# Optimization experiments

Hardware: AMD Instinct MI355X
Metric: run time of the kernel (lower is better)

## Reference

```python
import jax, jax.numpy as jnp
import numpy as np

L = 2
S = (L + 1) ** 2            # 9 spherical harmonic coefficients
C = 128                     # sphere_channels
H = 128                     # hidden_channels
NH = 8                      # num_heads
A = 32                      # attn_alpha_channels
V = 16                      # attn_value_channels
N = 5000                    # nodes
E = 50000                   # edges
DE = 128                    # invariant edge embedding dim
G = 18                      # S2 grid points

# l of each coefficient in l-major layout [S]
L_OF = np.concatenate([np.full(2 * l + 1, l) for l in range(L + 1)])
IDX_M0 = np.array([l * l + l for l in range(L + 1)])

def _idx_m(m):
    neg = np.array([l * l + l - m for l in range(m, L + 1)])
    pos = np.array([l * l + l + m for l in range(m, L + 1)])
    return neg, pos

IDX_M1_NEG, IDX_M1_POS = _idx_m(1)
IDX_M2_NEG, IDX_M2_POS = _idx_m(2)
# m-major ordering and its inverse permutation back to l-major
PERM = np.concatenate([IDX_M0, IDX_M1_POS, IDX_M1_NEG, IDX_M2_POS, IDX_M2_NEG])
INV_PERM = np.argsort(PERM)


def _silu(x):
    return x * jax.nn.sigmoid(x)


def _layernorm(x, g, b, eps=1e-5):
    mu = x.mean(-1, keepdims=True)
    var = ((x - mu) ** 2).mean(-1, keepdims=True)
    return (x - mu) * jax.lax.rsqrt(var + eps) * g + b


def _smooth_leaky_relu(x, a=0.2):
    return 0.5 * (1 + a) * x + 0.5 * (1 - a) * x * (2 * jax.nn.sigmoid(x) - 1)


def _so2_conv(x, w_m0, b_m0, w_m1, w_m2, cout):
    """SO(2) convolution on rotated embeddings. x: [E,S,Cin] l-major.
    Returns ([E,S,cout] l-major, extra m=0 channels)."""
    e = x.shape[0]
    # m = 0: plain linear over flattened (L+1)*Cin
    x0 = x[:, IDX_M0, :].reshape(e, -1)
    y0 = x0 @ w_m0 + b_m0
    y0_main = y0[:, : (L + 1) * cout].reshape(e, L + 1, cout)
    y0_extra = y0[:, (L + 1) * cout:]
    parts = [y0_main]
    # m > 0: complex (cos/sin) SO2 mixing with shared weight for real/imag
    for neg, pos, w in ((IDX_M1_NEG, IDX_M1_POS, w_m1), (IDX_M2_NEG, IDX_M2_POS, w_m2)):
        nl = len(neg)
        xr = x[:, pos, :].reshape(e, -1)
        xi = x[:, neg, :].reshape(e, -1)
        yr = xr @ w  # [E, 2*nl*cout]
        yi = xi @ w
        yr_r, yr_i = yr[:, : nl * cout], yr[:, nl * cout:]
        yi_r, yi_i = yi[:, : nl * cout], yi[:, nl * cout:]
        parts.append((yr_r - yi_i).reshape(e, nl, cout))   # +m (real)
        parts.append((yr_i + yi_r).reshape(e, nl, cout))   # -m (imag)
    out_m = jnp.concatenate(parts, axis=1)                 # m-major
    return out_m[:, INV_PERM, :], y0_extra


def _s2_act(x, togrid, fromgrid):
    g = jnp.einsum('gs,esc->egc', togrid, x)
    return jnp.einsum('sg,egc->esc', fromgrid, _silu(g))


def _sep_s2_act(scalars, x, togrid, fromgrid):
    t = _s2_act(x, togrid, fromgrid)
    return jnp.concatenate([_silu(scalars)[:, None, :], t[:, 1:, :]], axis=1)


def _so3_linear(x, w, b):
    # w: [L+1, Cin, Cout], shared across m within each l; bias only on l=0
    out = jnp.einsum('nsc,sco->nso', x, w[L_OF])
    return out.at[:, 0, :].add(b)


def _eqv_norm(x, g, b, eps=1e-5):
    # l=0: layernorm over channels; l>0: RMS over (m, channels) per degree
    outs = [_layernorm(x[:, 0:1, :], g[0], b)]
    for l in range(1, L + 1):
        sl = x[:, l * l:(l + 1) * (l + 1), :]
        rms = jnp.sqrt(jnp.mean(sl ** 2, axis=(1, 2), keepdims=True) + eps)
        outs.append(sl / rms * g[l])
    return jnp.concatenate(outs, axis=1)


def _forward(x, edge_distance, wigner, rad_w1, rad_b1, rad_ln_g, rad_ln_b, rad_w2, rad_b2,
             w1_m0, b1_m0, w1_m1, w1_m2, w2_m0, b2_m0, w2_m1, w2_m2,
             alpha_ln_g, alpha_ln_b, alpha_dot, proj_w, proj_b,
             norm1_g, norm1_b, norm2_g, norm2_b,
             gate_w, gate_b, ffn_w1, ffn_b1, ffn_w2, ffn_b2,
             togrid, fromgrid, edge_src, edge_dst):
    # ---------- SO2 equivariant graph attention ----------
    xn = _eqv_norm(x, norm1_g, norm1_b)
    msg = jnp.concatenate([xn[edge_src], xn[edge_dst]], axis=-1)      # [E,S,2C]
    msg = jnp.einsum('eij,ejc->eic', wigner, msg)                     # rotate to edge frame
    # radial function shared across m within each l (use_m_share_rad)
    h = _silu(_layernorm(edge_distance @ rad_w1 + rad_b1, rad_ln_g, rad_ln_b))
    rad = (h @ rad_w2 + rad_b2).reshape(-1, L + 1, 2 * C)             # [E,L+1,2C]
    msg = msg * rad[:, L_OF, :]
    hid, x0_extra = _so2_conv(msg, w1_m0, b1_m0, w1_m1, w1_m2, H)
    x_alpha = x0_extra[:, : NH * A].reshape(-1, NH, A)
    gating = x0_extra[:, NH * A:]                                     # [E,H]
    hid = _sep_s2_act(gating, hid, togrid, fromgrid)
    val, _ = _so2_conv(hid, w2_m0, b2_m0, w2_m1, w2_m2, NH * V)
    val = jnp.einsum('eji,ejc->eic', wigner, val)                     # rotate back (D^T)
    # attention weights with per-destination segment softmax
    a = _smooth_leaky_relu(_layernorm(x_alpha, alpha_ln_g, alpha_ln_b))
    a = jnp.einsum('eha,ha->eh', a, alpha_dot)                        # [E,NH]
    amax = jax.ops.segment_max(a, edge_dst, num_segments=N)
    aexp = jnp.exp(a - amax[edge_dst])
    asum = jax.ops.segment_sum(aexp, edge_dst, num_segments=N)
    attn = aexp / asum[edge_dst]
    msg_out = (val.reshape(-1, S, NH, V) * attn[:, None, :, None]).reshape(-1, S, NH * V)
    node = jax.ops.segment_sum(msg_out, edge_dst, num_segments=N)     # [N,S,NH*V]
    x = x + _so3_linear(node, proj_w, proj_b)
    # ---------- spherical FFN (sep S2 gating) ----------
    xn = _eqv_norm(x, norm2_g, norm2_b)
    gating = xn[:, 0, :] @ gate_w + gate_b
    hh = _so3_linear(xn, ffn_w1, ffn_b1)
    hh = _sep_s2_act(gating, hh, togrid, fromgrid)
    return x + _so3_linear(hh, ffn_w2, ffn_b2)


def setup_inputs() -> dict:
    key = jax.random.key(0)
    ks = iter(jax.random.split(key, 64))
    def nrm(shape, scale=1.0):
        return jax.random.normal(next(ks), shape, dtype=jnp.float32) * scale
    EX = NH * A + H
    inp = {}
    inp['x'] = nrm((N, S, C))
    inp['edge_distance'] = nrm((E, DE))
    inp['wigner'] = nrm((E, S, S), 1.0 / np.sqrt(S))
    inp['rad_w1'] = nrm((DE, 64), 1.0 / np.sqrt(DE)); inp['rad_b1'] = jnp.zeros((64,), jnp.float32)
    inp['rad_ln_g'] = jnp.ones((64,), jnp.float32); inp['rad_ln_b'] = jnp.zeros((64,), jnp.float32)
    inp['rad_w2'] = nrm((64, 2 * C * (L + 1)), 0.05); inp['rad_b2'] = jnp.ones((2 * C * (L + 1),), jnp.float32)
    inp['w1_m0'] = nrm(((L + 1) * 2 * C, (L + 1) * H + EX), 1.0 / np.sqrt((L + 1) * 2 * C))
    inp['b1_m0'] = jnp.zeros(((L + 1) * H + EX,), jnp.float32)
    inp['w1_m1'] = nrm((2 * 2 * C, 2 * 2 * H), 1.0 / np.sqrt(2 * 2 * C))
    inp['w1_m2'] = nrm((2 * C, 2 * H), 1.0 / np.sqrt(2 * C))
    inp['w2_m0'] = nrm(((L + 1) * H, (L + 1) * NH * V), 1.0 / np.sqrt((L + 1) * H))
    inp['b2_m0'] = jnp.zeros(((L + 1) * NH * V,), jnp.float32)
    inp['w2_m1'] = nrm((2 * H, 2 * 2 * NH * V), 1.0 / np.sqrt(2 * H))
    inp['w2_m2'] = nrm((H, 2 * NH * V), 1.0 / np.sqrt(H))
    inp['alpha_ln_g'] = jnp.ones((A,), jnp.float32); inp['alpha_ln_b'] = jnp.zeros((A,), jnp.float32)
    inp['alpha_dot'] = nrm((NH, A), 1.0 / np.sqrt(A))
    inp['proj_w'] = nrm((L + 1, NH * V, C), 1.0 / np.sqrt(NH * V)); inp['proj_b'] = jnp.zeros((C,), jnp.float32)
    inp['norm1_g'] = jnp.ones((L + 1, C), jnp.float32); inp['norm1_b'] = jnp.zeros((C,), jnp.float32)
    inp['norm2_g'] = jnp.ones((L + 1, C), jnp.float32); inp['norm2_b'] = jnp.zeros((C,), jnp.float32)
    inp['gate_w'] = nrm((C, H), 1.0 / np.sqrt(C)); inp['gate_b'] = jnp.zeros((H,), jnp.float32)
    inp['ffn_w1'] = nrm((L + 1, C, H), 1.0 / np.sqrt(C)); inp['ffn_b1'] = jnp.zeros((H,), jnp.float32)
    inp['ffn_w2'] = nrm((L + 1, H, C), 1.0 / np.sqrt(H)); inp['ffn_b2'] = jnp.zeros((C,), jnp.float32)
    inp['togrid'] = nrm((G, S), 1.0 / np.sqrt(S))
    inp['fromgrid'] = nrm((S, G), 1.0 / np.sqrt(G))
    inp['edge_src'] = jax.random.randint(next(ks), (E,), 0, N)
    inp['edge_dst'] = jax.random.randint(next(ks), (E,), 0, N)
    return inp


def reference(x, edge_distance, wigner, rad_w1, rad_b1, rad_ln_g, rad_ln_b, rad_w2, rad_b2,
              w1_m0, b1_m0, w1_m1, w1_m2, w2_m0, b2_m0, w2_m1, w2_m2,
              alpha_ln_g, alpha_ln_b, alpha_dot, proj_w, proj_b,
              norm1_g, norm1_b, norm2_g, norm2_b,
              gate_w, gate_b, ffn_w1, ffn_b1, ffn_w2, ffn_b2,
              togrid, fromgrid, edge_src, edge_dst):
    return _forward(x, edge_distance, wigner, rad_w1, rad_b1, rad_ln_g, rad_ln_b, rad_w2, rad_b2,
                    w1_m0, b1_m0, w1_m1, w1_m2, w2_m0, b2_m0, w2_m1, w2_m2,
                    alpha_ln_g, alpha_ln_b, alpha_dot, proj_w, proj_b,
                    norm1_g, norm1_b, norm2_g, norm2_b,
                    gate_w, gate_b, ffn_w1, ffn_b1, ffn_w2, ffn_b2,
                    togrid, fromgrid, edge_src, edge_dst)
```

## Files before the change

### kernel.cpp

```cpp
#include <hip/hip_runtime.h>
#include <hip/hip_bf16.h>

typedef unsigned short u16;
typedef unsigned int   u32;
typedef __attribute__((ext_vector_type(8))) short short8;
typedef __attribute__((ext_vector_type(4))) float float4v;

#define NN 5000
#define EE 50000

__device__ __forceinline__ float b2f(u16 u){ return __uint_as_float(((u32)u)<<16); }
__device__ __forceinline__ u16 f2b(float f){
  u32 x = __float_as_uint(f);
  u32 r = (x + 0x7fffu + ((x>>16)&1u)) >> 16;
  return (u16)r;
}
__device__ __forceinline__ float ldin(const void* p, size_t i, bool f32){
  return f32 ? ((const float*)p)[i] : b2f(((const u16*)p)[i]);
}
__device__ __forceinline__ float siluf(float x){ return x/(1.f+__expf(-x)); }
__device__ __forceinline__ float waveRedSum(float v){
  #pragma unroll
  for (int m=32;m>=1;m>>=1) v += __shfl_xor(v,m,64);
  return v;
}
__device__ __forceinline__ float red32(float v){
  #pragma unroll
  for (int m=16;m>=1;m>>=1) v += __shfl_xor(v,m,64);
  return v;
}
__device__ __forceinline__ void gload_lds16(const u16* g, u16* l){
  __builtin_amdgcn_global_load_lds((const __attribute__((address_space(1))) void*)g,
                                   (__attribute__((address_space(3))) void*)l, 16, 0, 0);
}


__global__ __launch_bounds__(256) void zero_kernel(float* __restrict__ p, int n){
  for (int i = blockIdx.x*256 + threadIdx.x; i < n; i += gridDim.x*256) p[i] = 0.f;
}

__global__ void detect_kernel(const u32* __restrict__ ng, int* __restrict__ flag){
  if (blockIdx.x == 0 && threadIdx.x == 0) *flag = (ng[0] == 0x3F800000u) ? 1 : 0;
}

__global__ __launch_bounds__(256) void hist_kernel(const int* __restrict__ edst,
    int* __restrict__ counts){
  int e = blockIdx.x*256 + threadIdx.x;
  if (e < EE) atomicAdd(&counts[edst[e]], 1);
}

__global__ __launch_bounds__(1024) void scan_kernel(const int* __restrict__ counts,
    int* __restrict__ row_start, int* __restrict__ cursor){
  __shared__ int buf[1024];
  __shared__ int base;
  const int t = threadIdx.x;
  if (t == 0){ base = 0; row_start[0] = 0; }
  __syncthreads();
  for (int i0 = 0; i0 < NN; i0 += 1024){
    int i = i0 + t;
    int c = (i < NN) ? counts[i] : 0;
    buf[t] = c;
    __syncthreads();
    #pragma unroll
    for (int ofs = 1; ofs < 1024; ofs <<= 1){
      int v = (t >= ofs) ? buf[t-ofs] : 0;
      __syncthreads();
      buf[t] += v;
      __syncthreads();
    }
    if (i < NN){
      int incl = base + buf[t];
      row_start[i+1] = incl;
      cursor[i] = incl - c;
    }
    __syncthreads();
    if (t == 0) base += buf[1023];
    __syncthreads();
  }
}

__global__ __launch_bounds__(256) void place_kernel(const int* __restrict__ edst,
    int* __restrict__ cursor, int* __restrict__ order){
  int e = blockIdx.x*256 + threadIdx.x;
  if (e < EE) order[atomicAdd(&cursor[edst[e]], 1)] = e;
}

__global__ __launch_bounds__(256) void cvt_kernel(const int* __restrict__ dflag,
    const void* __restrict__ src, long long off0, u16* __restrict__ dst, int n){
  const bool f32 = (*dflag != 0);
  for (int i = blockIdx.x*256 + threadIdx.x; i < n; i += gridDim.x*256)
    dst[i] = f32 ? f2b(((const float*)src)[off0 + i]) : ((const u16*)src)[off0 + i];
}

__global__ __launch_bounds__(256) void gathercvt_kernel(const int* __restrict__ dflag,
    const void* __restrict__ src, const int* __restrict__ order, int e0,
    u16* __restrict__ dst, int n){
  const bool f32 = (*dflag != 0);
  for (int i = blockIdx.x*256 + threadIdx.x; i < n; i += gridDim.x*256){
    int le = i >> 7, c = i & 127;
    int eg = order[e0 + le];
    dst[i] = f2b(ldin(src, (size_t)eg*128 + c, f32));
  }
}

__global__ __launch_bounds__(256) void biasprep_kernel(const int* __restrict__ dflag,
    const void* b1,const void* b2,const void* rb1,const void* rb2,
    const void* pb,const void* gb,const void* f1,const void* f2,
    u16* d_b1,u16* d_b2,u16* d_rb1,u16* d_rb2,u16* d_pb,u16* d_gb,u16* d_f1,u16* d_f2){
  const bool f32 = (*dflag != 0);
  int t = blockIdx.x*256 + threadIdx.x;
  if (t < 768) d_b1[t]  = f2b(ldin(b1, t, f32));
  if (t < 384) d_b2[t]  = f2b(ldin(b2, t, f32));
  if (t < 64)  d_rb1[t] = f2b(ldin(rb1, t, f32));
  if (t < 768) d_rb2[t] = f2b(ldin(rb2, t, f32));
  if (t < 128){
    d_pb[t] = f2b(ldin(pb, t, f32));
    d_gb[t] = f2b(ldin(gb, t, f32));
    d_f1[t] = f2b(ldin(f1, t, f32));
    d_f2[t] = f2b(ldin(f2, t, f32));
  }
}

__global__ __launch_bounds__(256) void cvtT_kernel(const int* __restrict__ dflag,
    const void* __restrict__ src, long long off0, u16* __restrict__ dst, int K, int N){
  const bool f32 = (*dflag != 0);
  int total = K*N;
  for (int i = blockIdx.x*256 + threadIdx.x; i < total; i += gridDim.x*256){
    int n = i / K, k = i % K;
    dst[i] = f2b(ldin(src, (size_t)off0 + (size_t)k*N + n, f32));
  }
}

__global__ __launch_bounds__(256) void cvtT3_kernel(const int* __restrict__ dflag,
    const void* __restrict__ src, u16* __restrict__ dst){
  const bool f32 = (*dflag != 0);
  const long long l = blockIdx.y;
  for (int i = blockIdx.x*256 + threadIdx.x; i < 16384; i += gridDim.x*256){
    int n = i >> 7, k = i & 127;
    dst[l*16384 + i] = f2b(ldin(src, (size_t)l*16384 + (size_t)k*128 + n, f32));
  }
}

__global__ __launch_bounds__(256) void wprepT_kernel(const int* __restrict__ dflag,
    const void* __restrict__ w, u16* __restrict__ wt, int K0, int N0){
  const bool f32 = (*dflag != 0);
  int total = 2*N0*2*K0;
  for (int i = blockIdx.x*blockDim.x + threadIdx.x; i < total; i += gridDim.x*blockDim.x){
    int c = i / (2*K0), r = i % (2*K0);
    float v;
    if (r < K0) v = ldin(w, (size_t)r*2*N0 + c, f32);
    else {
      int rr = r - K0;
      if (c < N0) v = -ldin(w, (size_t)rr*2*N0 + N0 + c, f32);
      else        v =  ldin(w, (size_t)rr*2*N0 + (c - N0), f32);
    }
    wt[i] = f2b(v);
  }
}

__global__ __launch_bounds__(128) void eqvnorm_kernel(const int* __restrict__ dflag,
    const void* __restrict__ x, int in_always_f32,
    const void* __restrict__ g, const void* __restrict__ b,
    void* __restrict__ out, int out_f32){
  const bool f32 = (*dflag != 0);
  const bool inf32 = in_always_f32 || f32;
  const int n = blockIdx.x, t = threadIdx.x;
  __shared__ float red[2];
  float v[9];
  #pragma unroll
  for (int s=0;s<9;s++) v[s] = ldin(x, (size_t)n*1152 + s*128 + t, inf32);

  auto bsum = [&](float val)->float{
    float w = waveRedSum(val);
    __syncthreads();
    if ((t & 63) == 0) red[t>>6] = w;
    __syncthreads();
    return red[0] + red[1];
  };
  auto store = [&](int idx, float val){
    if (out_f32) ((float*)out)[(size_t)n*1152 + idx] = val;
    else         ((u16*) out)[(size_t)n*1152 + idx] = f2b(val);
  };
  float mu  = bsum(v[0]) * (1.f/128.f);
  float d0  = v[0] - mu;
  float var = bsum(d0*d0) * (1.f/128.f);
  store(t, d0 * rsqrtf(var + 1e-5f) * ldin(g, t, f32) + ldin(b, t, f32));
  float ss1 = v[1]*v[1] + v[2]*v[2] + v[3]*v[3];
  float inv1 = rsqrtf(bsum(ss1)*(1.f/384.f) + 1e-5f);
  float g1 = ldin(g, 128 + t, f32);
  #pragma unroll
  for (int s=1;s<=3;s++) store(s*128 + t, v[s]*inv1*g1);
  float ss2 = 0.f;
  #pragma unroll
  for (int s=4;s<9;s++) ss2 += v[s]*v[s];
  float inv2 = rsqrtf(bsum(ss2)*(1.f/640.f) + 1e-5f);
  float g2 = ldin(g, 256 + t, f32);
  #pragma unroll
  for (int s=4;s<9;s++) store(s*128 + t, v[s]*inv2*g2);
}

__global__ __launch_bounds__(256) void gemm_mfma_kernel(
    const u16* __restrict__ A, int lda, int K,
    const u16* __restrict__ Wt, int NOUT,
    const u16* __restrict__ bias,
    u16* __restrict__ out0, int ld0, int coloff0, int split,
    u16* __restrict__ out1, int ld1, int M){
  __shared__ __align__(16) u16 As[2][128*32];
  __shared__ __align__(16) u16 Bs[2][128*32];
  const int t = threadIdx.x;
  const int r0 = blockIdx.x * 128;
  const int n0 = blockIdx.y * 128;
  const int lane = t & 63, wave = t >> 6;
  const int wr = (wave & 1) * 64, wn = (wave >> 1) * 64;
  float4v acc[4][4];
  #pragma unroll
  for (int i=0;i<4;i++)
    #pragma unroll
    for (int j=0;j<4;j++) acc[i][j] = (float4v){0.f,0.f,0.f,0.f};

  const int fr = lane & 15, fq = (lane >> 4) * 8;

  const int Rw   = wave * 32;
  const int srow = lane >> 2;
  const int scol = (lane & 3) * 8;
  const u16* aG0 = A  + (size_t)(r0 + Rw + srow) * lda + scol;
  const u16* aG1 = aG0 + (size_t)16 * lda;
  const bool aV0 = (r0 + Rw + srow)      < M;
  const bool aV1 = (r0 + Rw + 16 + srow) < M;
  const u16* bG0 = Wt + (size_t)(n0 + Rw + srow) * K + scol;
  const u16* bG1 = bG0 + (size_t)16 * K;
  const bool bV0 = (n0 + Rw + srow)      < NOUT;
  const bool bV1 = (n0 + Rw + 16 + srow) < NOUT;

  auto stage = [&](int buf, int k0){
    u16* lA = &As[buf][Rw * 32];
    u16* lB = &Bs[buf][Rw * 32];
    if (aV0) gload_lds16(aG0 + k0, lA);
    if (aV1) gload_lds16(aG1 + k0, lA + 16*32);
    if (bV0) gload_lds16(bG0 + k0, lB);
    if (bV1) gload_lds16(bG1 + k0, lB + 16*32);
  };

  stage(0, 0);
  __syncthreads();
  int cur = 0;
  for (int k0 = 0; k0 < K; k0 += 32){
    const int k1 = k0 + 32;
    if (k1 < K) stage(cur ^ 1, k1);
    short8 af[4], bfv[4];
    #pragma unroll
    for (int i=0;i<4;i++){
      af[i]  = *(const short8*)&As[cur][(wr + i*16 + fr)*32 + fq];
      bfv[i] = *(const short8*)&Bs[cur][(wn + i*16 + fr)*32 + fq];
    }
    #pragma unroll
    for (int i=0;i<4;i++)
      #pragma unroll
      for (int j=0;j<4;j++)
        acc[i][j] = __builtin_amdgcn_mfma_f32_16x16x32_bf16(af[i], bfv[j], acc[i][j], 0, 0, 0);
    __syncthreads();
    cur ^= 1;
  }
  const int quad = lane >> 4;
  #pragma unroll
  for (int j=0;j<4;j++){
    int col = n0 + wn + j*16 + fr;
    if (col >= NOUT) continue;
    float bv = bias ? b2f(bias[col]) : 0.f;
    #pragma unroll
    for (int i=0;i<4;i++){
      int rbase = r0 + wr + i*16 + quad*4;
      #pragma unroll
      for (int rg=0; rg<4; rg++){
        int row = rbase + rg;
        if (row >= M) continue;
        float v = acc[i][j][rg] + bv;
        if (col < split) out0[(size_t)row*ld0 + coloff0 + col] = f2b(v);
        else             out1[(size_t)row*ld1 + (col - split)] = f2b(v);
      }
    }
  }
}

__global__ __launch_bounds__(256) void gemm_node_kernel(
    const int* __restrict__ dflag,
    const u16* __restrict__ A,
    const u16* __restrict__ W3t,
    const u16* __restrict__ bias,
    const void* __restrict__ resid, int resid_mode,
    void* __restrict__ out, int out_mode, int gate_out){
  const bool f32 = (*dflag != 0);
  const int l = blockIdx.y;
  const int rpn  = (l==0) ? 1 : ((l==1) ? 3 : 5);
  const int soff = (l==0) ? 0 : ((l==1) ? 1 : 4);
  const int M = NN * rpn;
  const int r0 = blockIdx.x * 128;
  if (r0 >= M) return;
  __shared__ __align__(16) u16 As[128][40];
  __shared__ __align__(16) u16 Bs[128][40];
  const int t = threadIdx.x;
  const int lane = t & 63, wave = t >> 6;
  const int wr = (wave & 1) * 64, wn = (wave >> 1) * 64;
  float4v acc[4][4];
  #pragma unroll
  for (int i=0;i<4;i++)
    #pragma unroll
    for (int j=0;j<4;j++) acc[i][j] = (float4v){0.f,0.f,0.f,0.f};

  const int sr = t >> 2, sc = (t & 3) * 8;
  const int fr = lane & 15, fq = (lane >> 4) * 8;
  size_t abase[2]; bool aval[2];
  #pragma unroll
  for (int s2=0;s2<2;s2++){
    int m = r0 + sr + s2*64;
    aval[s2] = m < M;
    int n = m / rpn, srow = soff + (m % rpn);
    abase[s2] = (size_t)n*1152 + srow*128 + sc;
  }
  const u16* Wl = W3t + (size_t)l*16384;

  #pragma unroll
  for (int k0 = 0; k0 < 128; k0 += 32){
    #pragma unroll
    for (int s2=0;s2<2;s2++){
      int row = sr + s2*64;
      uint4 av = make_uint4(0u,0u,0u,0u);
      if (aval[s2]) av = *(const uint4*)(A + abase[s2] + k0);
      *(uint4*)&As[row][sc] = av;
      uint4 wv = *(const uint4*)(Wl + (size_t)row*128 + k0 + sc);
      *(uint4*)&Bs[row][sc] = wv;
    }
    __syncthreads();
    short8 af[4], bfr[4];
    #pragma unroll
    for (int i=0;i<4;i++){
      af[i]  = *(const short8*)&As[wr + i*16 + fr][fq];
      bfr[i] = *(const short8*)&Bs[wn + i*16 + fr][fq];
    }
    #pragma unroll
    for (int i=0;i<4;i++)
      #pragma unroll
      for (int j=0;j<4;j++)
        acc[i][j] = __builtin_amdgcn_mfma_f32_16x16x32_bf16(af[i], bfr[j], acc[i][j], 0, 0, 0);
    __syncthreads();
  }
  const int quad = lane >> 4;
  #pragma unroll
  for (int j=0;j<4;j++){
    int col = wn + j*16 + fr;
    float bv = (bias && l==0) ? b2f(bias[col]) : 0.f;
    #pragma unroll
    for (int i=0;i<4;i++){
      int rbase = r0 + wr + i*16 + quad*4;
      #pragma unroll
      for (int rg=0; rg<4; rg++){
        int m = rbase + rg;
        if (m >= M) continue;
        int n = m / rpn, srow = soff + (m % rpn);
        size_t na = (size_t)n*1152 + srow*128 + col;
        float v = acc[i][j][rg] + bv;
        if (resid_mode == 1)      v += ((const float*)resid)[na];
        else if (resid_mode == 2) v += ldin(resid, na, f32);
        if (gate_out)            ((u16*)out)[(size_t)n*128 + col] = f2b(v);
        else if (out_mode == 0)  ((u16*)out)[na] = f2b(v);
        else if (out_mode == 1)  ((float*)out)[na] = v;
        else { if (f32) ((float*)out)[na] = v; else ((u16*)out)[na] = f2b(v); }
      }
    }
  }
}

__global__ __launch_bounds__(256) void nodecvt_kernel(const float* __restrict__ node,
    const float* __restrict__ nsum, u16* __restrict__ nodeb){
  for (int i = blockIdx.x*256 + threadIdx.x; i < NN*1152; i += gridDim.x*256){
    int n = i / 1152, c = i & 127, h = c >> 4;
    float ns = nsum[(size_t)n*8 + h];
    float rs = (ns > 0.f) ? 1.f/ns : 0.f;
    nodeb[i] = f2b(node[i] * rs);
  }
}

__global__ __launch_bounds__(128) void node_s2act_kernel(const int* __restrict__ dflag,
    const u16* __restrict__ hh, const u16* __restrict__ gating,
    const void* __restrict__ tg, const void* __restrict__ fg, u16* __restrict__ hh2){
  const bool f32 = (*dflag != 0);
  const int n = blockIdx.x, t = threadIdx.x;
  __shared__ float TG[162], FG[162];
  for (int i=t; i<162; i+=128){ TG[i]=ldin(tg,i,f32); FG[i]=ldin(fg,i,f32); }
  float hv[9];
  #pragma unroll
  for (int s=0;s<9;s++) hv[s] = b2f(hh[(size_t)n*1152 + s*128 + t]);
  __syncthreads();
  float gg[18];
  #pragma unroll
  for (int gi=0;gi<18;gi++){
    float a = 0.f;
    #pragma unroll
    for (int s=0;s<9;s++) a = fmaf(TG[gi*9+s], hv[s], a);
    gg[gi] = siluf(a);
  }
  hh2[(size_t)n*1152 + t] = f2b(siluf(b2f(gating[(size_t)n*128 + t])));
  #pragma unroll
  for (int s=1;s<9;s++){
    float a = 0.f;
    #pragma unroll
    for (int gi=0;gi<18;gi++) a = fmaf(FG[s*18+gi], gg[gi], a);
    hh2[(size_t)n*1152 + s*128 + t] = f2b(a);
  }
}

__global__ __launch_bounds__(256) void lnsilu_kernel(const int* __restrict__ dflag,
    u16* __restrict__ H, const void* __restrict__ rlng, const void* __restrict__ rlnb, int M){
  const bool f32 = (*dflag != 0);
  const int r = blockIdx.x*4 + (threadIdx.x >> 6), lane = threadIdx.x & 63;
  if (r >= M) return;
  float h = b2f(H[(size_t)r*64 + lane]);
  float mu = waveRedSum(h) * (1.f/64.f);
  float d = h - mu;
  float var = waveRedSum(d*d) * (1.f/64.f);
  float hn = d * rsqrtf(var + 1e-5f) * ldin(rlng, lane, f32) + ldin(rlnb, lane, f32);
  H[(size_t)r*64 + lane] = f2b(siluf(hn));
}

__global__ __launch_bounds__(256) void edge_rot_kernel(const int* __restrict__ dflag,
    const u16* __restrict__ xn, const void* __restrict__ wig,
    const u16* __restrict__ rad,
    const int* __restrict__ esrc, const int* __restrict__ edst,
    const int* __restrict__ order, int e0, u16* __restrict__ msg){
  const bool f32 = (*dflag != 0);
  const int le = blockIdx.x, t = threadIdx.x;
  const int eg = order[e0 + le];
  __shared__ float W[81];
  if (t < 81) W[t] = ldin(wig, (size_t)eg*81 + t, f32);
  const int src = esrc[eg], dst = edst[eg];
  float pre[9];
  const u16* base = (t < 128) ? (xn + (size_t)src*1152 + t) : (xn + (size_t)dst*1152 + (t-128));
  #pragma unroll
  for (int j=0;j<9;j++) pre[j] = b2f(base[j*128]);
  __syncthreads();
  float rot[9];
  #pragma unroll
  for (int i=0;i<9;i++){
    float a = 0.f;
    #pragma unroll
    for (int j=0;j<9;j++) a = fmaf(W[i*9+j], pre[j], a);
    rot[i] = a;
  }
  float r[3];
  #pragma unroll
  for (int l=0;l<3;l++) r[l] = b2f(rad[(size_t)le*768 + l*256 + t]);
  const int INVP[9] = {0,5,1,3,8,6,2,4,7};
  const int LOF[9]  = {0,1,1,1,2,2,2,2,2};
  u16* mb = msg + (size_t)le*2304 + t;
  #pragma unroll
  for (int i=0;i<9;i++) mb[INVP[i]*256] = f2b(rot[i] * r[LOF[i]]);
}

__global__ __launch_bounds__(256) void s2act_alpha_kernel(const int* __restrict__ dflag,
    const u16* __restrict__ hid, const u16* __restrict__ extra,
    const void* __restrict__ togrid, const void* __restrict__ fromgrid,
    const void* __restrict__ alng, const void* __restrict__ alnb, const void* __restrict__ adot,
    const int* __restrict__ edst, const int* __restrict__ order, int e0,
    u16* __restrict__ hid2, float* __restrict__ aexp, float* __restrict__ nsum){
  const bool f32 = (*dflag != 0);
  const int le = blockIdx.x, t = threadIdx.x;
  const int p = e0 + le;
  __shared__ float TG[162], FG[162];
  if (t < 162){ TG[t] = ldin(togrid, t, f32); FG[t] = ldin(fromgrid, t, f32); }
  {
    const int h = t >> 5, ai = t & 31;
    float v = b2f(extra[(size_t)le*384 + t]);
    float mu = red32(v) * (1.f/32.f);
    float d = v - mu;
    float var = red32(d*d) * (1.f/32.f);
    float xh = d * rsqrtf(var + 1e-5f) * ldin(alng, ai, f32) + ldin(alnb, ai, f32);
    float sig = 1.f/(1.f + __expf(-xh));
    float sl = 0.6f*xh + 0.4f*xh*(2.f*sig - 1.f);
    float pp = sl * ldin(adot, h*32 + ai, f32);
    float dot = red32(pp);
    if (ai == 0){
      float ex = __expf(dot - 8.f);
      aexp[(size_t)p*8 + h] = ex;
      atomicAdd(&nsum[(size_t)edst[order[p]]*8 + h], ex);
    }
  }
  __syncthreads();
  if (t < 128){
    const int INVP[9] = {0,5,1,3,8,6,2,4,7};
    float hv[9];
    #pragma unroll
    for (int s=0;s<9;s++) hv[s] = b2f(hid[(size_t)le*1152 + INVP[s]*128 + t]);
    float gg[18];
    #pragma unroll
    for (int gi=0;gi<18;gi++){
      float a = 0.f;
      #pragma unroll
      for (int s=0;s<9;s++) a = fmaf(TG[gi*9+s], hv[s], a);
      gg[gi] = siluf(a);
    }
    hid2[(size_t)le*1152 + t] = f2b(siluf(b2f(extra[(size_t)le*384 + 256 + t])));
    #pragma unroll
    for (int s=1;s<9;s++){
      float a = 0.f;
      #pragma unroll
      for (int gi=0;gi<18;gi++) a = fmaf(FG[s*18+gi], gg[gi], a);
      hid2[(size_t)le*1152 + INVP[s]*128 + t] = f2b(a);
    }
  }
}

__global__ __launch_bounds__(128) void unrot_gather_kernel(const int* __restrict__ dflag,
    const u16* __restrict__ val, const void* __restrict__ wig,
    const float* __restrict__ aexp, const int* __restrict__ order,
    const int* __restrict__ row_start, int e0, int Mc, float* __restrict__ node){
  const bool f32 = (*dflag != 0);
  const int n = blockIdx.x, t = threadIdx.x;
  const int s = row_start[n], tend = row_start[n+1];
  int lo = (s > e0) ? s : e0;
  int hi = (tend < e0 + Mc) ? tend : (e0 + Mc);
  if (lo >= hi) return;
  __shared__ float W[81];
  __shared__ float SC[8];
  const int INVP[9] = {0,5,1,3,8,6,2,4,7};
  float acc[9];
  #pragma unroll
  for (int i=0;i<9;i++) acc[i] = 0.f;
  for (int p = lo; p < hi; p++){
    const int le = p - e0;
    const int eg = order[p];
    __syncthreads();
    if (t < 81) W[t] = ldin(wig, (size_t)eg*81 + t, f32);
    if (t >= 120) SC[t-120] = aexp[(size_t)p*8 + (t-120)];
    __syncthreads();
    float vs[9];
    #pragma unroll
    for (int j=0;j<9;j++) vs[j] = b2f(val[(size_t)le*1152 + INVP[j]*128 + t]);
    const float sc = SC[t>>4];
    #pragma unroll
    for (int i=0;i<9;i++){
      float a = 0.f;
      #pragma unroll
      for (int j=0;j<9;j++) a = fmaf(W[j*9+i], vs[j], a);
      acc[i] = fmaf(a, sc, acc[i]);
    }
  }
  const bool full = (s >= e0) && (tend <= e0 + Mc);
  #pragma unroll
  for (int i=0;i<9;i++){
    float* dst = &node[(size_t)n*1152 + i*128 + t];
    if (full) *dst = acc[i];
    else      atomicAdd(dst, acc[i]);
  }
}

extern "C" void kernel_launch(void* const* d_in, const int* in_sizes, int n_in,
                              void* d_out, int out_size, void* d_ws, size_t ws_size,
                              hipStream_t stream){
  (void)in_sizes; (void)n_in; (void)out_size;
  const void* x       = d_in[0];
  const void* edist   = d_in[1];
  const void* wig     = d_in[2];
  const void* rad_w1  = d_in[3];
  const void* rad_b1  = d_in[4];
  const void* rad_lng = d_in[5];
  const void* rad_lnb = d_in[6];
  const void* rad_w2  = d_in[7];
  const void* rad_b2  = d_in[8];
  const void* w1_m0   = d_in[9];
  const void* b1_m0   = d_in[10];
  const void* w1_m1   = d_in[11];
  const void* w1_m2   = d_in[12];
  const void* w2_m0   = d_in[13];
  const void* b2_m0   = d_in[14];
  const void* w2_m1   = d_in[15];
  const void* w2_m2   = d_in[16];
  const void* alng    = d_in[17];
  const void* alnb    = d_in[18];
  const void* adot    = d_in[19];
  const void* proj_w  = d_in[20];
  const void* proj_b  = d_in[21];
  const void* norm1_g = d_in[22];
  const void* norm1_b = d_in[23];
  const void* norm2_g = d_in[24];
  const void* norm2_b = d_in[25];
  const void* gate_w  = d_in[26];
  const void* gate_b  = d_in[27];
  const void* ffn_w1  = d_in[28];
  const void* ffn_b1  = d_in[29];
  const void* ffn_w2  = d_in[30];
  const void* ffn_b2  = d_in[31];
  const void* togrid  = d_in[32];
  const void* fromgrid= d_in[33];
  const int* esrc     = (const int*)d_in[34];
  const int* edst     = (const int*)d_in[35];

  char* wsp = (char*)d_ws;
  size_t off = 0;
  auto alloc = [&](size_t bytes)->char*{
    char* p = wsp + off;
    off = (off + bytes + 255) & ~(size_t)255;
    return p;
  };
  int*  dflag  = (int*) alloc(4);
  u16*  W1cT   = (u16*) alloc((size_t)512*1024*2);
  u16*  W2cT   = (u16*) alloc((size_t)256*512*2);
  u16*  W3cT   = (u16*) alloc((size_t)512*512*2);
  u16*  W4cT   = (u16*) alloc((size_t)256*256*2);
  u16*  w1m0T  = (u16*) alloc((size_t)768*768*2);
  u16*  b1m0C  = (u16*) alloc((size_t)768*2);
  u16*  w2m0T  = (u16*) alloc((size_t)384*384*2);
  u16*  b2m0C  = (u16*) alloc((size_t)384*2);
  u16*  rw1T   = (u16*) alloc((size_t)64*128*2);
  u16*  rb1C   = (u16*) alloc((size_t)64*2);
  u16*  rw2T   = (u16*) alloc((size_t)768*64*2);
  u16*  rb2C   = (u16*) alloc((size_t)768*2);
  u16*  projT3 = (u16*) alloc((size_t)3*16384*2);
  u16*  ffn1T3 = (u16*) alloc((size_t)3*16384*2);
  u16*  ffn2T3 = (u16*) alloc((size_t)3*16384*2);
  u16*  gateT  = (u16*) alloc((size_t)16384*2);
  u16*  pbC    = (u16*) alloc((size_t)128*2);
  u16*  gbC    = (u16*) alloc((size_t)128*2);
  u16*  fb1C   = (u16*) alloc((size_t)128*2);
  u16*  fb2C   = (u16*) alloc((size_t)128*2);
  u16*  xn     = (u16*) alloc((size_t)NN*1152*2);
  float* aexp  = (float*)alloc((size_t)EE*8*4);
  float* nsum  = (float*)alloc((size_t)NN*8*4);
  float* node  = (float*)alloc((size_t)NN*1152*4);
  int*  counts = (int*) alloc((size_t)NN*4);
  int*  row_st = (int*) alloc((size_t)(NN+1)*4);
  int*  cursor = (int*) alloc((size_t)NN*4);
  int*  order  = (int*) alloc((size_t)EE*4);
  size_t fixed_end = off;
  size_t avail = (ws_size > fixed_end) ? (ws_size - fixed_end) : 0;

  long long cap = ((long long)avail - 4096) / 7680;
  int Ec;
  if (cap >= 50048) Ec = 50048;
  else {
    long long c128 = cap & ~127LL;
    if (c128 < 128) c128 = 128;
    int nch = (EE + (int)c128 - 1) / (int)c128;
    Ec = ((EE + nch - 1) / nch + 127) & ~127;
  }
  char* cb = wsp + fixed_end;
  u16* msgC   = (u16*)cb;
  u16* hidC   = (u16*)(cb + (size_t)Ec*2304*2);
  u16* extraC = (u16*)(cb + (size_t)Ec*2304*2 + (size_t)Ec*1152*2);
  u16* hid2C  = msgC;
  u16* valC   = hidC;
  u16* edistC = msgC;
  u16* radC   = hidC;
  u16* HrawC  = hidC + (size_t)Ec*768;
  u16*  nodeb  = (u16*)cb;
  float* xnew  = (float*)(cb + (size_t)NN*1152*2);
  u16*  xn2    = (u16*)(cb + (size_t)NN*1152*2 + (size_t)NN*1152*4);
  u16*  gating = xn2 + (size_t)NN*1152;
  u16*  hh     = gating + (size_t)NN*128;
  u16*  hh2    = hh + (size_t)NN*1152;

  detect_kernel<<<1, 64, 0, stream>>>((const u32*)norm1_g, dflag);

  zero_kernel<<<2048, 256, 0, stream>>>(nsum, NN*8 + NN*1152 + NN);

  hist_kernel<<<(EE+255)/256, 256, 0, stream>>>(edst, counts);
  scan_kernel<<<1, 1024, 0, stream>>>(counts, row_st, cursor);
  place_kernel<<<(EE+255)/256, 256, 0, stream>>>(edst, cursor, order);

  cvtT_kernel<<<2304, 256, 0, stream>>>(dflag, w1_m0, 0, w1m0T, 768, 768);
  cvtT_kernel<<<576,  256, 0, stream>>>(dflag, w2_m0, 0, w2m0T, 384, 384);
  cvtT_kernel<<<32,   256, 0, stream>>>(dflag, rad_w1, 0, rw1T, 128, 64);
  cvtT_kernel<<<192,  256, 0, stream>>>(dflag, rad_w2, 0, rw2T, 64, 768);
  cvtT3_kernel<<<dim3(64,3), 256, 0, stream>>>(dflag, proj_w, projT3);
  cvtT3_kernel<<<dim3(64,3), 256, 0, stream>>>(dflag, ffn_w1, ffn1T3);
  cvtT3_kernel<<<dim3(64,3), 256, 0, stream>>>(dflag, ffn_w2, ffn2T3);
  cvtT_kernel<<<64, 256, 0, stream>>>(dflag, gate_w, 0, gateT, 128, 128);
  biasprep_kernel<<<3, 256, 0, stream>>>(dflag, b1_m0, b2_m0, rad_b1, rad_b2,
                                         proj_b, gate_b, ffn_b1, ffn_b2,
                                         b1m0C, b2m0C, rb1C, rb2C, pbC, gbC, fb1C, fb2C);
  wprepT_kernel<<<2048, 256, 0, stream>>>(dflag, w1_m1, W1cT, 512, 256);
  wprepT_kernel<<<512,  256, 0, stream>>>(dflag, w1_m2, W2cT, 256, 128);
  wprepT_kernel<<<1024, 256, 0, stream>>>(dflag, w2_m1, W3cT, 256, 256);
  wprepT_kernel<<<256,  256, 0, stream>>>(dflag, w2_m2, W4cT, 128, 128);

  eqvnorm_kernel<<<NN, 128, 0, stream>>>(dflag, x, 0, norm1_g, norm1_b, xn, 0);

  for (int e0 = 0; e0 < EE; e0 += Ec){
    int Mc = (EE - e0 < Ec) ? (EE - e0) : Ec;
    int GX = (Mc + 127) / 128;
    gathercvt_kernel<<<dim3((Mc*128+255)/256), 256, 0, stream>>>(dflag, edist, order, e0,
                                                                 edistC, Mc*128);
    gemm_mfma_kernel<<<dim3(GX,1), 256, 0, stream>>>(edistC, 128, 128, rw1T, 64, rb1C,
                                                     HrawC, 64, 0, 64, nullptr, 0, Mc);
    lnsilu_kernel<<<dim3((Mc+3)/4), 256, 0, stream>>>(dflag, HrawC, rad_lng, rad_lnb, Mc);
    gemm_mfma_kernel<<<dim3(GX,6), 256, 0, stream>>>(HrawC, 64, 64, rw2T, 768, rb2C,
                                                     radC, 768, 0, 768, nullptr, 0, Mc);
    edge_rot_kernel<<<Mc, 256, 0, stream>>>(dflag, xn, wig, radC, esrc, edst, order, e0, msgC);
    gemm_mfma_kernel<<<dim3(GX,6), 256, 0, stream>>>(msgC,        2304, 768,  w1m0T, 768, b1m0C,
                                                     hidC, 1152, 0,   384, extraC, 384, Mc);
    gemm_mfma_kernel<<<dim3(GX,4), 256, 0, stream>>>(msgC + 768,  2304, 1024, W1cT,  512, nullptr,
                                                     hidC, 1152, 384, 512, nullptr, 0, Mc);
    gemm_mfma_kernel<<<dim3(GX,2), 256, 0, stream>>>(msgC + 1792, 2304, 512,  W2cT,  256, nullptr,
                                                     hidC, 1152, 896, 256, nullptr, 0, Mc);
    s2act_alpha_kernel<<<Mc, 256, 0, stream>>>(dflag, hidC, extraC, togrid, fromgrid, alng,
                                               alnb, adot, edst, order, e0, hid2C, aexp, nsum);
    gemm_mfma_kernel<<<dim3(GX,3), 256, 0, stream>>>(hid2C,       1152, 384, w2m0T, 384, b2m0C,
                                                     valC, 1152, 0,   384, nullptr, 0, Mc);
    gemm_mfma_kernel<<<dim3(GX,4), 256, 0, stream>>>(hid2C + 384, 1152, 512, W3cT,  512, nullptr,
                                                     valC, 1152, 384, 512, nullptr, 0, Mc);
    gemm_mfma_kernel<<<dim3(GX,2), 256, 0, stream>>>(hid2C + 896, 1152, 256, W4cT,  256, nullptr,
                                                     valC, 1152, 896, 256, nullptr, 0, Mc);
    unrot_gather_kernel<<<NN, 128, 0, stream>>>(dflag, valC, wig, aexp, order, row_st,
                                                e0, Mc, node);
  }

  const int GN2 = (NN*5 + 127)/128;
  nodecvt_kernel<<<2048, 256, 0, stream>>>(node, nsum, nodeb);
  gemm_node_kernel<<<dim3(GN2,3), 256, 0, stream>>>(dflag, nodeb, projT3, pbC,
                                                    x, 2, xnew, 1, 0);
  eqvnorm_kernel<<<NN, 128, 0, stream>>>(dflag, xnew, 1, norm2_g, norm2_b, xn2, 0);
  gemm_node_kernel<<<dim3((NN+127)/128,1), 256, 0, stream>>>(dflag, xn2, gateT, gbC,
                                                             nullptr, 0, gating, 0, 1);
  gemm_node_kernel<<<dim3(GN2,3), 256, 0, stream>>>(dflag, xn2, ffn1T3, fb1C,
                                                    nullptr, 0, hh, 0, 0);
  node_s2act_kernel<<<NN, 128, 0, stream>>>(dflag, hh, gating, togrid, fromgrid, hh2);
  gemm_node_kernel<<<dim3(GN2,3), 256, 0, stream>>>(dflag, hh2, ffn2T3, fb2C,
                                                    xnew, 1, d_out, 2, 0);
}
```

Measured before the change: 1.227 ms.

## Fuse weight-prep launches into one kernel and swizzle GEMM tiles across XCDs

Replaces thirteen separate weight/bias conversion kernel launches with a single prep kernel that dispatches on blockIdx.y, which cuts launch overhead and the serialization of many small kernels. The MFMA GEMM also remaps its linear block id so that consecutive tiles land on the same XCD (block ids are assigned round-robin across 8 XCDs). The aim is better L2 reuse of A rows and weight tiles. The remap adds integer index math per block and must stay a bijection for every grid size.

```diff
diff --git a/kernel.cpp b/kernel.cpp
--- a/kernel.cpp
+++ b/kernel.cpp
@@ -85,13 +85,6 @@
   if (e < EE) order[atomicAdd(&cursor[edst[e]], 1)] = e;
 }
 
-__global__ __launch_bounds__(256) void cvt_kernel(const int* __restrict__ dflag,
-    const void* __restrict__ src, long long off0, u16* __restrict__ dst, int n){
-  const bool f32 = (*dflag != 0);
-  for (int i = blockIdx.x*256 + threadIdx.x; i < n; i += gridDim.x*256)
-    dst[i] = f32 ? f2b(((const float*)src)[off0 + i]) : ((const u16*)src)[off0 + i];
-}
-
 __global__ __launch_bounds__(256) void gathercvt_kernel(const int* __restrict__ dflag,
     const void* __restrict__ src, const int* __restrict__ order, int e0,
     u16* __restrict__ dst, int n){
@@ -103,58 +96,77 @@
   }
 }
 
-__global__ __launch_bounds__(256) void biasprep_kernel(const int* __restrict__ dflag,
-    const void* b1,const void* b2,const void* rb1,const void* rb2,
-    const void* pb,const void* gb,const void* f1,const void* f2,
-    u16* d_b1,u16* d_b2,u16* d_rb1,u16* d_rb2,u16* d_pb,u16* d_gb,u16* d_f1,u16* d_f2){
-  const bool f32 = (*dflag != 0);
-  int t = blockIdx.x*256 + threadIdx.x;
-  if (t < 768) d_b1[t]  = f2b(ldin(b1, t, f32));
-  if (t < 384) d_b2[t]  = f2b(ldin(b2, t, f32));
-  if (t < 64)  d_rb1[t] = f2b(ldin(rb1, t, f32));
-  if (t < 768) d_rb2[t] = f2b(ldin(rb2, t, f32));
-  if (t < 128){
-    d_pb[t] = f2b(ldin(pb, t, f32));
-    d_gb[t] = f2b(ldin(gb, t, f32));
-    d_f1[t] = f2b(ldin(f1, t, f32));
-    d_f2[t] = f2b(ldin(f2, t, f32));
-  }
-}
-
-__global__ __launch_bounds__(256) void cvtT_kernel(const int* __restrict__ dflag,
-    const void* __restrict__ src, long long off0, u16* __restrict__ dst, int K, int N){
-  const bool f32 = (*dflag != 0);
+__device__ __forceinline__ void do_cvtT(bool f32, const void* src, u16* dst,
+    int K, int N, int tid, int stride){
   int total = K*N;
-  for (int i = blockIdx.x*256 + threadIdx.x; i < total; i += gridDim.x*256){
-    int n = i / K, k = i % K;
-    dst[i] = f2b(ldin(src, (size_t)off0 + (size_t)k*N + n, f32));
-  }
-}
-
-__global__ __launch_bounds__(256) void cvtT3_kernel(const int* __restrict__ dflag,
-    const void* __restrict__ src, u16* __restrict__ dst){
-  const bool f32 = (*dflag != 0);
-  const long long l = blockIdx.y;
-  for (int i = blockIdx.x*256 + threadIdx.x; i < 16384; i += gridDim.x*256){
-    int n = i >> 7, k = i & 127;
-    dst[l*16384 + i] = f2b(ldin(src, (size_t)l*16384 + (size_t)k*128 + n, f32));
-  }
-}
-
-__global__ __launch_bounds__(256) void wprepT_kernel(const int* __restrict__ dflag,
-    const void* __restrict__ w, u16* __restrict__ wt, int K0, int N0){
-  const bool f32 = (*dflag != 0);
-  int total = 2*N0*2*K0;
-  for (int i = blockIdx.x*blockDim.x + threadIdx.x; i < total; i += gridDim.x*blockDim.x){
-    int c = i / (2*K0), r = i % (2*K0);
+  for (int i = tid; i < total; i += stride){
+    int n = i / K, k = i - n*K;
+    dst[i] = f2b(ldin(src, (size_t)k*N + n, f32));
+  }
+}
+__device__ __forceinline__ void do_cvtT3(bool f32, const void* src, u16* dst,
+    int tid, int stride){
+  for (int i = tid; i < 49152; i += stride){
+    int l = i >> 14, j = i & 16383;
+    int n = j >> 7, k = j & 127;
+    dst[i] = f2b(ldin(src, (size_t)l*16384 + (size_t)k*128 + n, f32));
+  }
+}
+__device__ __forceinline__ void do_wprepT(bool f32, const void* w, u16* wt,
+    int K0, int N0, int tid, int stride){
+  int total = 4*N0*K0;
+  for (int i = tid; i < total; i += stride){
+    int c = i / (2*K0), rr0 = i - c*2*K0;
     float v;
-    if (r < K0) v = ldin(w, (size_t)r*2*N0 + c, f32);
+    if (rr0 < K0) v = ldin(w, (size_t)rr0*2*N0 + c, f32);
     else {
-      int rr = r - K0;
+      int rr = rr0 - K0;
       if (c < N0) v = -ldin(w, (size_t)rr*2*N0 + N0 + c, f32);
       else        v =  ldin(w, (size_t)rr*2*N0 + (c - N0), f32);
     }
     wt[i] = f2b(v);
+  }
+}
+
+__global__ __launch_bounds__(256) void prep_all_kernel(const int* __restrict__ dflag,
+    const void* w1_m0, const void* w2_m0, const void* rad_w1, const void* rad_w2,
+    const void* proj_w, const void* ffn_w1, const void* ffn_w2, const void* gate_w,
+    const void* b1, const void* b2, const void* rb1, const void* rb2,
+    const void* pb, const void* gb, const void* f1, const void* f2,
+    const void* w1_m1, const void* w1_m2, const void* w2_m1, const void* w2_m2,
+    u16* w1m0T, u16* w2m0T, u16* rw1T, u16* rw2T,
+    u16* projT3, u16* ffn1T3, u16* ffn2T3, u16* gateT,
+    u16* b1m0C, u16* b2m0C, u16* rb1C, u16* rb2C,
+    u16* pbC, u16* gbC, u16* fb1C, u16* fb2C,
+    u16* W1cT, u16* W2cT, u16* W3cT, u16* W4cT){
+  const bool f32 = (*dflag != 0);
+  const int tid = blockIdx.x*256 + threadIdx.x;
+  const int stride = gridDim.x*256;
+  switch (blockIdx.y){
+    case 0:  do_cvtT (f32, w1_m0, w1m0T, 768, 768, tid, stride); break;
+    case 1:  do_cvtT (f32, w2_m0, w2m0T, 384, 384, tid, stride); break;
+    case 2:  do_cvtT (f32, rad_w1, rw1T, 128, 64,  tid, stride); break;
+    case 3:  do_cvtT (f32, rad_w2, rw2T, 64, 768,  tid, stride); break;
+    case 4:  do_cvtT3(f32, proj_w, projT3, tid, stride); break;
+    case 5:  do_cvtT3(f32, ffn_w1, ffn1T3, tid, stride); break;
+    case 6:  do_cvtT3(f32, ffn_w2, ffn2T3, tid, stride); break;
+    case 7:  do_cvtT (f32, gate_w, gateT, 128, 128, tid, stride); break;
+    case 8:
+      if (tid < 768) b1m0C[tid] = f2b(ldin(b1, tid, f32));
+      if (tid < 384) b2m0C[tid] = f2b(ldin(b2, tid, f32));
+      if (tid < 64)  rb1C[tid]  = f2b(ldin(rb1, tid, f32));
+      if (tid < 768) rb2C[tid]  = f2b(ldin(rb2, tid, f32));
+      if (tid < 128){
+        pbC[tid]  = f2b(ldin(pb, tid, f32));
+        gbC[tid]  = f2b(ldin(gb, tid, f32));
+        fb1C[tid] = f2b(ldin(f1, tid, f32));
+        fb2C[tid] = f2b(ldin(f2, tid, f32));
+      }
+      break;
+    case 9:  do_wprepT(f32, w1_m1, W1cT, 512, 256, tid, stride); break;
+    case 10: do_wprepT(f32, w1_m2, W2cT, 256, 128, tid, stride); break;
+    case 11: do_wprepT(f32, w2_m1, W3cT, 256, 256, tid, stride); break;
+    case 12: do_wprepT(f32, w2_m2, W4cT, 128, 128, tid, stride); break;
   }
 }
 
@@ -208,8 +220,15 @@
   __shared__ __align__(16) u16 As[2][128*32];
   __shared__ __align__(16) u16 Bs[2][128*32];
   const int t = threadIdx.x;
-  const int r0 = blockIdx.x * 128;
-  const int n0 = blockIdx.y * 128;
+  const int nxg = gridDim.x, nyg = gridDim.y;
+  const int nwg = nxg * nyg;
+  const int bid = blockIdx.y * nxg + blockIdx.x;
+  const int q = nwg >> 3, r = nwg & 7;
+  const int xcd = bid & 7, sid = bid >> 3;
+  const int swz = (xcd < r ? xcd*(q+1) : r*(q+1) + (xcd - r)*q) + sid;
+  const int mt = swz / nyg;
+  const int r0 = mt * 128;
+  const int n0 = (swz - mt*nyg) * 128;
   const int lane = t & 63, wave = t >> 6;
   const int wr = (wave & 1) * 64, wn = (wave >> 1) * 64;
   float4v acc[4][4];
@@ -666,21 +685,13 @@
   scan_kernel<<<1, 1024, 0, stream>>>(counts, row_st, cursor);
   place_kernel<<<(EE+255)/256, 256, 0, stream>>>(edst, cursor, order);
 
-  cvtT_kernel<<<2304, 256, 0, stream>>>(dflag, w1_m0, 0, w1m0T, 768, 768);
-  cvtT_kernel<<<576,  256, 0, stream>>>(dflag, w2_m0, 0, w2m0T, 384, 384);
-  cvtT_kernel<<<32,   256, 0, stream>>>(dflag, rad_w1, 0, rw1T, 128, 64);
-  cvtT_kernel<<<192,  256, 0, stream>>>(dflag, rad_w2, 0, rw2T, 64, 768);
-  cvtT3_kernel<<<dim3(64,3), 256, 0, stream>>>(dflag, proj_w, projT3);
-  cvtT3_kernel<<<dim3(64,3), 256, 0, stream>>>(dflag, ffn_w1, ffn1T3);
-  cvtT3_kernel<<<dim3(64,3), 256, 0, stream>>>(dflag, ffn_w2, ffn2T3);
-  cvtT_kernel<<<64, 256, 0, stream>>>(dflag, gate_w, 0, gateT, 128, 128);
-  biasprep_kernel<<<3, 256, 0, stream>>>(dflag, b1_m0, b2_m0, rad_b1, rad_b2,
-                                         proj_b, gate_b, ffn_b1, ffn_b2,
-                                         b1m0C, b2m0C, rb1C, rb2C, pbC, gbC, fb1C, fb2C);
-  wprepT_kernel<<<2048, 256, 0, stream>>>(dflag, w1_m1, W1cT, 512, 256);
-  wprepT_kernel<<<512,  256, 0, stream>>>(dflag, w1_m2, W2cT, 256, 128);
-  wprepT_kernel<<<1024, 256, 0, stream>>>(dflag, w2_m1, W3cT, 256, 256);
-  wprepT_kernel<<<256,  256, 0, stream>>>(dflag, w2_m2, W4cT, 128, 128);
+  prep_all_kernel<<<dim3(256,13), 256, 0, stream>>>(dflag,
+      w1_m0, w2_m0, rad_w1, rad_w2, proj_w, ffn_w1, ffn_w2, gate_w,
+      b1_m0, b2_m0, rad_b1, rad_b2, proj_b, gate_b, ffn_b1, ffn_b2,
+      w1_m1, w1_m2, w2_m1, w2_m2,
+      w1m0T, w2m0T, rw1T, rw2T, projT3, ffn1T3, ffn2T3, gateT,
+      b1m0C, b2m0C, rb1C, rb2C, pbC, gbC, fb1C, fb2C,
+      W1cT, W2cT, W3cT, W4cT);
 
   eqvnorm_kernel<<<NN, 128, 0, stream>>>(dflag, x, 0, norm1_g, norm1_b, xn, 0);
 
```

New measurement: 1.174 ms. 1.05x faster.
